# Optimization experiments

Measured on AMD Instinct MI355X. Metric: run time of the kernel, lower is better.

Reference implementation:

```python
import jax, jax.numpy as jnp
import numpy as np

B, C, H, W = 32, 3, 224, 224
P = 16
D = 768
NH = 12
HD = D // NH
DFF = 3072
L = 12
MAXLEN = 256
S = (H // P) * (W // P)  # 196 patches
EPS = 1e-5


def setup_inputs() -> dict:
    key = jax.random.key(0)
    ks = jax.random.split(key, 10)
    r = lambda k, shp, s=0.02: jax.random.normal(k, shp, jnp.float32) * s
    return {
        "x": jax.random.normal(ks[0], (B, C, H, W), jnp.float32),
        "bn_gamma": jnp.ones((C,), jnp.float32),
        "bn_beta": jnp.zeros((C,), jnp.float32),
        "bn_mean": jnp.zeros((C,), jnp.float32),
        "bn_var": jnp.ones((C,), jnp.float32),
        "proj_w": r(ks[1], (P * P * 3, D)),
        "proj_b": jnp.zeros((D,), jnp.float32),
        "cls_w": r(ks[2], (1, D)),
        "Wq": r(ks[3], (L, D, D)),
        "Wk": r(ks[4], (L, D, D)),
        "Wv": r(ks[5], (L, D, D)),
        "fc1_w": r(ks[6], (L, D, DFF)),
        "fc1_b": jnp.zeros((L, DFF), jnp.float32),
        "fc2_w": r(ks[7], (L, DFF, D)),
        "fc2_b": jnp.zeros((L, D), jnp.float32),
        "ln1_g": jnp.ones((L, D), jnp.float32),
        "ln1_b": jnp.zeros((L, D), jnp.float32),
        "ln2_g": jnp.ones((L, D), jnp.float32),
        "ln2_b": jnp.zeros((L, D), jnp.float32),
    }


def _pos_encoding(max_len, d):
    # Faithful to source: exponent is 2*i/d where i is the EVEN index itself.
    pos = jnp.arange(max_len, dtype=jnp.float32)[:, None]
    i = jnp.arange(0, d, 2, dtype=jnp.float32)[None, :]
    ang = pos / (10000.0 ** (2.0 * i / d))
    pe = jnp.zeros((max_len, d), jnp.float32)
    pe = pe.at[:, 0::2].set(jnp.sin(ang))
    pe = pe.at[:, 1::2].set(jnp.cos(ang))
    return pe


def _layernorm(x, g, b):
    m = jnp.mean(x, axis=-1, keepdims=True)
    v = jnp.mean((x - m) ** 2, axis=-1, keepdims=True)
    return (x - m) * jax.lax.rsqrt(v + EPS) * g + b


def reference(x, bn_gamma, bn_beta, bn_mean, bn_var, proj_w, proj_b, cls_w,
              Wq, Wk, Wv, fc1_w, fc1_b, fc2_w, fc2_b,
              ln1_g, ln1_b, ln2_g, ln2_b):
    b = x.shape[0]
    # BatchNorm2d (inference mode, running stats)
    xb = (x - bn_mean[None, :, None, None]) * jax.lax.rsqrt(bn_var[None, :, None, None] + EPS)
    xb = xb * bn_gamma[None, :, None, None] + bn_beta[None, :, None, None]
    # Patchify (nn.Unfold order: channel-major within each patch) -> [B, S, C*P*P]
    patches = xb.reshape(b, C, H // P, P, W // P, P)
    patches = patches.transpose(0, 2, 4, 1, 3, 5).reshape(b, S, C * P * P)
    h = patches @ proj_w + proj_b  # [B, S, D]
    cls = jnp.broadcast_to(cls_w[None], (b, 1, D))
    h = jnp.concatenate([cls, h], axis=1)  # [B, S+1, D]
    pe = _pos_encoding(MAXLEN, D)
    h = h + pe[None, : S + 1, :]
    scale = 1.0 / jnp.sqrt(jnp.float32(HD))
    n = S + 1
    for l in range(L):
        q = (h @ Wq[l]).reshape(b, n, NH, HD).transpose(0, 2, 1, 3)
        k = (h @ Wk[l]).reshape(b, n, NH, HD).transpose(0, 2, 1, 3)
        v = (h @ Wv[l]).reshape(b, n, NH, HD).transpose(0, 2, 1, 3)
        scores = jnp.einsum("bhqd,bhkd->bhqk", q, k) * scale
        attn = jax.nn.softmax(scores, axis=-1)
        att = jnp.einsum("bhqk,bhkd->bhqd", attn, v)  # [B, NH, n, HD]
        # Source bug replicated: direct view [B,NH,n,HD] -> [B,n,D] (no head transpose)
        att = att.reshape(b, n, D)
        h1 = _layernorm(h + att, ln1_g[l], ln1_b[l])
        ff = jax.nn.relu(h1 @ fc1_w[l] + fc1_b[l]) @ fc2_w[l] + fc2_b[l]
        h = _layernorm(h1 + ff, ln2_g[l], ln2_b[l])
    return h[:, 0, :]
```

## Files before the change

### kernel.cpp

```cpp
#include <hip/hip_runtime.h>

typedef unsigned short u16;
typedef __bf16 bf16x8 __attribute__((ext_vector_type(8)));
typedef float f32x4 __attribute__((ext_vector_type(4)));

#define NB 32
#define ND 768
#define NTOK 197
#define NROWS (NB * NTOK)
#define NPATCH 196
#define PROWS (NB * NPATCH)
#define NHD 12
#define NDFF 3072
#define NLAY 12
#define NQKV 2304

static __device__ __forceinline__ u16 f2b(float f) {
  unsigned int u = __builtin_bit_cast(unsigned int, f);
  unsigned int r = u + 0x7FFFu + ((u >> 16) & 1u);
  return (u16)(r >> 16);
}

static __device__ __forceinline__ float wsum(float v) {
#pragma unroll
  for (int off = 32; off > 0; off >>= 1) v += __shfl_xor(v, off);
  return v;
}

static __device__ __forceinline__ void stage16(const u16* g, u16* l) {
  __builtin_amdgcn_global_load_lds((const __attribute__((address_space(1))) void*)g,
                                   (__attribute__((address_space(3))) void*)l, 16, 0, 0);
}

__global__ void pe_kernel(float* __restrict__ pe) {
  int idx = blockIdx.x * 256 + threadIdx.x;
  if (idx >= NTOK * ND) return;
  int t = idx / ND, d = idx % ND;
  int i = d & ~1;
  float e = (2.0f * (float)i) / (float)ND;
  float denom = powf(10000.0f, e);
  float ang = (float)t / denom;
  pe[idx] = (d & 1) ? cosf(ang) : sinf(ang);
}

__global__ void patch_kernel(const float* __restrict__ x,
                             const float* __restrict__ bng, const float* __restrict__ bnb,
                             const float* __restrict__ bnm, const float* __restrict__ bnv,
                             u16* __restrict__ out) {
  int idx = blockIdx.x * 256 + threadIdx.x;
  if (idx >= PROWS * ND) return;
  int row = idx / ND, col = idx % ND;
  int b = row / NPATCH, s = row % NPATCH;
  int ph = s / 14, pw = s % 14;
  int c = col / 256, rr = col % 256;
  int py = rr / 16, px = rr % 16;
  float v = x[(((size_t)(b * 3 + c) * 224) + ph * 16 + py) * 224 + pw * 16 + px];
  v = (v - bnm[c]) * rsqrtf(bnv[c] + 1e-5f) * bng[c] + bnb[c];
  out[idx] = f2b(v);
}

__global__ void cls_kernel(const float* __restrict__ cls_w, const float* __restrict__ pe,
                           float* __restrict__ h, u16* __restrict__ hb) {
  int idx = blockIdx.x * 256 + threadIdx.x;
  if (idx >= NB * ND) return;
  int b = idx / ND, d = idx % ND;
  float v = cls_w[d] + pe[d];
  size_t o = (size_t)(b * NTOK) * ND + d;
  h[o] = v;
  hb[o] = f2b(v);
}

__global__ __launch_bounds__(256) void transpose_cvt(const float* __restrict__ src,
                                                     u16* __restrict__ dst, int R, int C) {
  __shared__ float tile[32][33];
  int tx = threadIdx.x, ty = threadIdx.y;
  int c0 = blockIdx.x * 32, r0 = blockIdx.y * 32;
#pragma unroll
  for (int i = ty; i < 32; i += 8) {
    int r = r0 + i, c = c0 + tx;
    tile[i][tx] = (r < R && c < C) ? src[(size_t)r * C + c] : 0.f;
  }
  __syncthreads();
#pragma unroll
  for (int i = ty; i < 32; i += 8) {
    int c = c0 + i, r = r0 + tx;
    if (r < R && c < C) dst[(size_t)c * R + r] = f2b(tile[tx][i]);
  }
}

__global__ __launch_bounds__(256) void transpose_layer(
    const float* __restrict__ Wq, const float* __restrict__ Wk, const float* __restrict__ Wv,
    const float* __restrict__ f1, const float* __restrict__ f2,
    u16* __restrict__ wqkvt, u16* __restrict__ fc1t, u16* __restrict__ fc2t) {
  int idx = blockIdx.x;
  const float* src;
  u16* dst;
  int C, R, rt, ct;
  if (idx < 1728) {
    int z = idx / 576, loc = idx % 576;
    src = z == 0 ? Wq : (z == 1 ? Wk : Wv);
    dst = wqkvt + (size_t)z * ND * ND;
    R = 768; C = 768; rt = loc / 24; ct = loc % 24;
  } else if (idx < 4032) {
    int loc = idx - 1728;
    src = f1; dst = fc1t; R = 768; C = 3072; rt = loc / 96; ct = loc % 96;
  } else {
    int loc = idx - 4032;
    src = f2; dst = fc2t; R = 3072; C = 768; rt = loc / 24; ct = loc % 24;
  }
  __shared__ float tile[32][33];
  int tx = threadIdx.x & 31, ty = threadIdx.x >> 5;
  int r0 = rt * 32, c0 = ct * 32;
#pragma unroll
  for (int i = ty; i < 32; i += 8) tile[i][tx] = src[(size_t)(r0 + i) * C + c0 + tx];
  __syncthreads();
#pragma unroll
  for (int i = ty; i < 32; i += 8) dst[(size_t)(c0 + i) * R + r0 + tx] = f2b(tile[tx][i]);
}

template <int MODE>
__global__ __launch_bounds__(512, 4) void gemm2(const u16* __restrict__ A,
                                                const u16* __restrict__ Bt,
                                                const float* __restrict__ bias,
                                                const float* __restrict__ pe,
                                                float* __restrict__ Cf, u16* __restrict__ Cb,
                                                int M, int N, int K, int lda, int nby) {
  __shared__ u16 smem[36864];
  const int tid = threadIdx.x;
  const int w = tid >> 6, l = tid & 63;
  const int lr = l & 15, lg = l >> 4;
  const int wr = w >> 1, wc = w & 1;

  const int nwg = gridDim.x;
  const int q8 = nwg >> 3, r8 = nwg & 7;
  const int xcd = blockIdx.x & 7, sidx = blockIdx.x >> 3;
  const int swz = (xcd < r8 ? xcd * (q8 + 1) : r8 * (q8 + 1) + (xcd - r8) * q8) + sidx;
  const int m0 = (swz / nby) * 256, n0 = (swz % nby) * 128;

  A += (size_t)blockIdx.z * K;
  Bt += (size_t)blockIdx.z * K;

  const int srow = l >> 2;
  const int scol = (((l & 3) ^ ((l >> 2) & 3) ^ ((l >> 4) & 3))) * 8;
  int raA0 = m0 + 32 * w + srow;
  int raA1 = raA0 + 16;
  raA0 = raA0 < M ? raA0 : M - 1;
  raA1 = raA1 < M ? raA1 : M - 1;
  const int rbB = n0 + 16 * w + srow;
  const u16* pA0 = A + (size_t)raA0 * lda + scol;
  const u16* pA1 = A + (size_t)raA1 * lda + scol;
  const u16* pB = Bt + (size_t)rbB * lda + scol;
  const int dsgA0 = (2 * w) * 512;
  const int dsgA1 = (2 * w + 1) * 512;
  const int dsgB = 8192 + w * 512;

  const int xo = ((lg ^ (lr & 3) ^ ((lr >> 2) & 3))) * 8;
  const int aoff = (wr * 64 + lr) * 32 + xo;
  const int boff = 8192 + (wc * 64 + lr) * 32 + xo;

  f32x4 acc[4][4] = {};
  const int nk = K >> 5;

#define BARF                           \
  {                                    \
    __builtin_amdgcn_sched_barrier(0); \
    __builtin_amdgcn_s_barrier();      \
    asm volatile("" ::: "memory");     \
    __builtin_amdgcn_sched_barrier(0); \
  }
#define VMW(N) asm volatile("s_waitcnt vmcnt(" #N ")" ::: "memory");

  stage16(pA0, smem + dsgA0);
  stage16(pA1, smem + dsgA1);
  stage16(pB, smem + dsgB);
  stage16(pA0 + 32, smem + 12288 + dsgA0);
  stage16(pA1 + 32, smem + 12288 + dsgA1);
  stage16(pB + 32, smem + 12288 + dsgB);
  VMW(3);
  BARF;

  int cur = 0;
  for (int t = 0; t < nk; ++t) {
    const u16* sb = smem + cur * 12288;
    int c2 = cur + 2;
    if (c2 >= 3) c2 -= 3;
    const bool more2 = (t + 2) < nk;
    if (more2) {
      u16* db = smem + c2 * 12288;
      const int ko = (t + 2) * 32;
      stage16(pA0 + ko, db + dsgA0);
      stage16(pA1 + ko, db + dsgA1);
      stage16(pB + ko, db + dsgB);
    }
    bf16x8 ar[4], br[4];
#pragma unroll
    for (int n = 0; n < 4; ++n) br[n] = *(const bf16x8*)(sb + boff + n * 512);
#pragma unroll
    for (int m = 0; m < 4; ++m) ar[m] = *(const bf16x8*)(sb + aoff + m * 512);
    __builtin_amdgcn_s_setprio(1);
#pragma unroll
    for (int m = 0; m < 4; ++m) {
#pragma unroll
      for (int n = 0; n < 4; ++n)
        acc[m][n] = __builtin_amdgcn_mfma_f32_16x16x32_bf16(ar[m], br[n], acc[m][n], 0, 0, 0);
    }
    __builtin_amdgcn_s_setprio(0);
    if (more2) {
      VMW(3);
    } else if (t + 1 < nk) {
      VMW(0);
    }
    if (t + 1 < nk) BARF;
    cur = cur == 2 ? 0 : cur + 1;
  }

  const size_t zoff = (size_t)blockIdx.z * (size_t)M * (size_t)N;
#pragma unroll
  for (int m = 0; m < 4; ++m) {
    const int rowb = m0 + wr * 64 + m * 16 + lg * 4;
#pragma unroll
    for (int n = 0; n < 4; ++n) {
      const int col = n0 + wc * 64 + n * 16 + lr;
      float bval = (MODE == 0 || MODE == 2) ? bias[col] : 0.f;
#pragma unroll
      for (int r = 0; r < 4; ++r) {
        const int row = rowb + r;
        if (row < M) {
          float v = acc[m][n][r] + bval;
          if (MODE == 2) v = fmaxf(v, 0.f);
          if (MODE == 0) {
            int b = row / NPATCH, t = 1 + row % NPATCH;
            float val = v + pe[(size_t)t * ND + col];
            size_t o = (size_t)(b * NTOK + t) * ND + col;
            Cf[o] = val;
            Cb[o] = f2b(val);
          } else if (MODE == 4) {
            Cf[zoff + (size_t)row * N + col] = v;
          } else {
            Cb[(size_t)row * N + col] = f2b(v);
          }
        }
      }
    }
  }
}

__global__ __launch_bounds__(256) void attn_kernel(const u16* __restrict__ qkv,
                                                   float* __restrict__ att) {
  const int b = blockIdx.x, h = blockIdx.y;
  const int tid = threadIdx.x;
  const int wave = tid >> 6, lane = tid & 63;
  const int lr = lane & 15, lg = lane >> 4;
  __shared__ u16 Vt[64][232];
  __shared__ u16 Pl[4][16][232];

  const size_t bbase = (size_t)(b * NTOK) * NQKV + h * 64;

  for (int idx = tid; idx < NTOK * 64; idx += 256) {
    int k2 = idx >> 6, d = idx & 63;
    Vt[d][k2] = qkv[bbase + (size_t)k2 * NQKV + 1536 + d];
  }
  for (int idx = tid; idx < 64 * 35; idx += 256) {
    int d = idx / 35, k2 = 197 + idx % 35;
    Vt[d][k2] = 0;
  }
  for (int idx = tid; idx < 4 * 16 * 24; idx += 256) {
    int w = idx / (16 * 24), rr = (idx / 24) % 16, c = 208 + idx % 24;
    Pl[w][rr][c] = 0;
  }
  __syncthreads();

  for (int mt = wave; mt < 13; mt += 4) {
    int qrow = mt * 16 + lr;
    if (qrow > 196) qrow = 196;
    bf16x8 af[2];
#pragma unroll
    for (int ks = 0; ks < 2; ks++)
      af[ks] =
          *reinterpret_cast<const bf16x8*>(qkv + bbase + (size_t)qrow * NQKV + ks * 32 + lg * 8);

    f32x4 sf[13];
#pragma unroll
    for (int nt = 0; nt < 13; nt++) {
      int krow = nt * 16 + lr;
      if (krow > 196) krow = 196;
      f32x4 z = {0.f, 0.f, 0.f, 0.f};
#pragma unroll
      for (int ks = 0; ks < 2; ks++) {
        bf16x8 bf_ = *reinterpret_cast<const bf16x8*>(qkv + bbase + (size_t)krow * NQKV + 768 +
                                                      ks * 32 + lg * 8);
        z = __builtin_amdgcn_mfma_f32_16x16x32_bf16(af[ks], bf_, z, 0, 0, 0);
      }
      sf[nt] = z;
    }

    float sm[4];
#pragma unroll
    for (int r = 0; r < 4; r++) {
      float mx = -1e30f;
#pragma unroll
      for (int nt = 0; nt < 13; nt++) {
        int col = nt * 16 + lr;
        float val = (col < NTOK) ? sf[nt][r] * 0.125f : -1e30f;
        sf[nt][r] = val;
        mx = fmaxf(mx, val);
      }
#pragma unroll
      for (int off = 1; off < 16; off <<= 1) mx = fmaxf(mx, __shfl_xor(mx, off));
      float sum = 0.f;
#pragma unroll
      for (int nt = 0; nt < 13; nt++) {
        float pv = __expf(sf[nt][r] - mx);
        sum += pv;
        Pl[wave][lg * 4 + r][nt * 16 + lr] = f2b(pv);
      }
#pragma unroll
      for (int off = 1; off < 16; off <<= 1) sum += __shfl_xor(sum, off);
      sm[r] = sum;
    }

#pragma unroll
    for (int dt = 0; dt < 4; dt++) {
      f32x4 o = {0.f, 0.f, 0.f, 0.f};
#pragma unroll
      for (int ks = 0; ks < 7; ks++) {
        bf16x8 pa = *reinterpret_cast<const bf16x8*>(&Pl[wave][lr][ks * 32 + lg * 8]);
        bf16x8 vv = *reinterpret_cast<const bf16x8*>(&Vt[dt * 16 + lr][ks * 32 + lg * 8]);
        o = __builtin_amdgcn_mfma_f32_16x16x32_bf16(pa, vv, o, 0, 0, 0);
      }
#pragma unroll
      for (int r = 0; r < 4; r++) {
        int q = mt * 16 + lg * 4 + r;
        if (q < NTOK)
          att[(size_t)b * (NTOK * ND) + ((size_t)(h * NTOK + q)) * 64 + dt * 16 + lr] =
              o[r] / sm[r];
      }
    }
  }
}

__global__ __launch_bounds__(256) void ln_kernel(const float* __restrict__ xa,
                                                 const float* __restrict__ xb,
                                                 const float* __restrict__ gw,
                                                 const float* __restrict__ bw,
                                                 float* __restrict__ yf, u16* __restrict__ yb) {
  int row = blockIdx.x, tid = threadIdx.x;
  size_t base = (size_t)row * ND;
  float v[3];
  float s = 0.f;
#pragma unroll
  for (int i = 0; i < 3; i++) {
    int d = tid + i * 256;
    v[i] = xa[base + d] + xb[base + d];
    s += v[i];
  }
  __shared__ float red[4];
  __shared__ float red2[4];
  s = wsum(s);
  if ((tid & 63) == 0) red[tid >> 6] = s;
  __syncthreads();
  float mean = (red[0] + red[1] + red[2] + red[3]) * (1.f / 768.f);
  float q = 0.f;
#pragma unroll
  for (int i = 0; i < 3; i++) {
    float d0 = v[i] - mean;
    q += d0 * d0;
  }
  q = wsum(q);
  if ((tid & 63) == 0) red2[tid >> 6] = q;
  __syncthreads();
  float inv = rsqrtf((red2[0] + red2[1] + red2[2] + red2[3]) * (1.f / 768.f) + 1e-5f);
#pragma unroll
  for (int i = 0; i < 3; i++) {
    int d = tid + i * 256;
    float val = (v[i] - mean) * inv * gw[d] + bw[d];
    yf[base + d] = val;
    yb[base + d] = f2b(val);
  }
}

__global__ __launch_bounds__(256) void ln_fuse2(const float* __restrict__ h1,
                                                const float* __restrict__ parts,
                                                const float* __restrict__ fb,
                                                const float* __restrict__ gw,
                                                const float* __restrict__ bw,
                                                float* __restrict__ yf, u16* __restrict__ yb) {
  const size_t PS = (size_t)NROWS * ND;
  int row = blockIdx.x, tid = threadIdx.x;
  size_t base = (size_t)row * ND;
  float v[3];
  float s = 0.f;
#pragma unroll
  for (int i = 0; i < 3; i++) {
    int d = tid + i * 256;
    v[i] = h1[base + d] + parts[base + d] + parts[PS + base + d] + parts[2 * PS + base + d] +
           fb[d];
    s += v[i];
  }
  __shared__ float red[4];
  __shared__ float red2[4];
  s = wsum(s);
  if ((tid & 63) == 0) red[tid >> 6] = s;
  __syncthreads();
  float mean = (red[0] + red[1] + red[2] + red[3]) * (1.f / 768.f);
  float q = 0.f;
#pragma unroll
  for (int i = 0; i < 3; i++) {
    float d0 = v[i] - mean;
    q += d0 * d0;
  }
  q = wsum(q);
  if ((tid & 63) == 0) red2[tid >> 6] = q;
  __syncthreads();
  float inv = rsqrtf((red2[0] + red2[1] + red2[2] + red2[3]) * (1.f / 768.f) + 1e-5f);
#pragma unroll
  for (int i = 0; i < 3; i++) {
    int d = tid + i * 256;
    float val = (v[i] - mean) * inv * gw[d] + bw[d];
    yf[base + d] = val;
    yb[base + d] = f2b(val);
  }
}

__global__ void outcopy_kernel(const float* __restrict__ h, float* __restrict__ out) {
  int idx = blockIdx.x * 256 + threadIdx.x;
  if (idx >= NB * ND) return;
  int b = idx / ND, d = idx % ND;
  out[idx] = h[(size_t)(b * NTOK) * ND + d];
}

extern "C" void kernel_launch(void* const* d_in, const int* in_sizes, int n_in, void* d_out,
                              int out_size, void* d_ws, size_t ws_size, hipStream_t stream) {
  const float* x = (const float*)d_in[0];
  const float* bng = (const float*)d_in[1];
  const float* bnb = (const float*)d_in[2];
  const float* bnm = (const float*)d_in[3];
  const float* bnv = (const float*)d_in[4];
  const float* proj_w = (const float*)d_in[5];
  const float* proj_b = (const float*)d_in[6];
  const float* cls_w = (const float*)d_in[7];
  const float* Wq = (const float*)d_in[8];
  const float* Wk = (const float*)d_in[9];
  const float* Wv = (const float*)d_in[10];
  const float* fc1_w = (const float*)d_in[11];
  const float* fc1_b = (const float*)d_in[12];
  const float* fc2_w = (const float*)d_in[13];
  const float* fc2_b = (const float*)d_in[14];
  const float* ln1_g = (const float*)d_in[15];
  const float* ln1_b = (const float*)d_in[16];
  const float* ln2_g = (const float*)d_in[17];
  const float* ln2_b = (const float*)d_in[18];

  char* wp = (char*)d_ws;
  auto carve = [&](size_t bytes) -> char* {
    char* r = wp;
    wp += (bytes + 255) & ~(size_t)255;
    return r;
  };
  float* pe = (float*)carve((size_t)NTOK * ND * 4);
  u16* patches = (u16*)carve((size_t)PROWS * ND * 2);
  u16* projwt = (u16*)carve((size_t)ND * ND * 2);
  u16* wqkvt = (u16*)carve((size_t)NQKV * ND * 2);
  u16* fc1t = (u16*)carve((size_t)ND * NDFF * 2);
  u16* fc2t = (u16*)carve((size_t)ND * NDFF * 2);
  float* h = (float*)carve((size_t)NROWS * ND * 4);
  u16* hb = (u16*)carve((size_t)NROWS * ND * 2);
  float* h1 = (float*)carve((size_t)NROWS * ND * 4);
  u16* h1b = (u16*)carve((size_t)NROWS * ND * 2);
  char* uni = carve(3 * (size_t)NROWS * ND * 4);
  u16* qkvb = (u16*)uni;
  float* parts = (float*)uni;
  float* att = (float*)carve((size_t)NROWS * ND * 4);
  u16* ffb = (u16*)carve((size_t)NROWS * NDFF * 2);
  if ((size_t)(wp - (char*)d_ws) > ws_size) return;

  pe_kernel<<<(NTOK * ND + 255) / 256, 256, 0, stream>>>(pe);
  patch_kernel<<<(PROWS * ND + 255) / 256, 256, 0, stream>>>(x, bng, bnb, bnm, bnv, patches);
  transpose_cvt<<<dim3(24, 24), dim3(32, 8), 0, stream>>>(proj_w, projwt, ND, ND);
  gemm2<0><<<dim3(150, 1, 1), 512, 0, stream>>>(patches, projwt, proj_b, pe, h, hb, PROWS, ND,
                                                ND, ND, 6);
  cls_kernel<<<(NB * ND + 255) / 256, 256, 0, stream>>>(cls_w, pe, h, hb);

  for (int l = 0; l < NLAY; ++l) {
    size_t wo = (size_t)l * ND * ND;
    transpose_layer<<<6336, 256, 0, stream>>>(Wq + wo, Wk + wo, Wv + wo,
                                              fc1_w + (size_t)l * ND * NDFF,
                                              fc2_w + (size_t)l * NDFF * ND, wqkvt, fc1t, fc2t);
    gemm2<1><<<dim3(450, 1, 1), 512, 0, stream>>>(hb, wqkvt, nullptr, nullptr, nullptr, qkvb,
                                                  NROWS, NQKV, ND, ND, 18);
    attn_kernel<<<dim3(NB, NHD), 256, 0, stream>>>(qkvb, att);
    ln_kernel<<<NROWS, 256, 0, stream>>>(h, att, ln1_g + l * ND, ln1_b + l * ND, h1, h1b);
    gemm2<2><<<dim3(600, 1, 1), 512, 0, stream>>>(h1b, fc1t, fc1_b + l * NDFF, nullptr, nullptr,
                                                  ffb, NROWS, NDFF, ND, ND, 24);
    gemm2<4><<<dim3(150, 1, 3), 512, 0, stream>>>(ffb, fc2t, nullptr, nullptr, parts, nullptr,
                                                  NROWS, ND, 1024, NDFF, 6);
    ln_fuse2<<<NROWS, 256, 0, stream>>>(h1, parts, fc2_b + l * ND, ln2_g + l * ND, ln2_b + l * ND,
                                        h, hb);
  }
  outcopy_kernel<<<(NB * ND + 255) / 256, 256, 0, stream>>>(h, (float*)d_out);
}
```

Baseline: 2.354 ms.

## Store attention output and split-K partials in bf16; vectorize patch, transpose, and layernorm kernels

Attention output and the three split-K FC2 partial sums are now written as bf16 instead of fp32, which halves their memory traffic. The layernorm kernels are rewritten to use 384 threads, each handling two elements with vector loads. The weight transpose now works on 64x64 tiles with float2 loads and packed bf16 stores, and the patch kernel produces 8 elements per thread. Rounding the split-K partials and the attention output to bf16 before summing adds numerical error.

```diff
diff --git a/kernel.cpp b/kernel.cpp
--- a/kernel.cpp
+++ b/kernel.cpp
@@ -1,8 +1,10 @@
 #include <hip/hip_runtime.h>
 
 typedef unsigned short u16;
+typedef unsigned int u32;
 typedef __bf16 bf16x8 __attribute__((ext_vector_type(8)));
 typedef float f32x4 __attribute__((ext_vector_type(4)));
+typedef u16 u16x8 __attribute__((ext_vector_type(8)));
 
 #define NB 32
 #define ND 768
@@ -16,9 +18,13 @@
 #define NQKV 2304
 
 static __device__ __forceinline__ u16 f2b(float f) {
-  unsigned int u = __builtin_bit_cast(unsigned int, f);
-  unsigned int r = u + 0x7FFFu + ((u >> 16) & 1u);
+  u32 u = __builtin_bit_cast(u32, f);
+  u32 r = u + 0x7FFFu + ((u >> 16) & 1u);
   return (u16)(r >> 16);
+}
+static __device__ __forceinline__ float b2f(u16 u) {
+  u32 x = ((u32)u) << 16;
+  return __builtin_bit_cast(float, x);
 }
 
 static __device__ __forceinline__ float wsum(float v) {
@@ -48,15 +54,20 @@
                              const float* __restrict__ bnm, const float* __restrict__ bnv,
                              u16* __restrict__ out) {
   int idx = blockIdx.x * 256 + threadIdx.x;
-  if (idx >= PROWS * ND) return;
-  int row = idx / ND, col = idx % ND;
+  if (idx >= PROWS * 96) return;
+  int row = idx / 96, c8 = (idx % 96) * 8;
   int b = row / NPATCH, s = row % NPATCH;
   int ph = s / 14, pw = s % 14;
-  int c = col / 256, rr = col % 256;
-  int py = rr / 16, px = rr % 16;
-  float v = x[(((size_t)(b * 3 + c) * 224) + ph * 16 + py) * 224 + pw * 16 + px];
-  v = (v - bnm[c]) * rsqrtf(bnv[c] + 1e-5f) * bng[c] + bnb[c];
-  out[idx] = f2b(v);
+  int c = c8 / 256, rr = c8 % 256;
+  int py = rr / 16, px0 = rr % 16;
+  const float* xp =
+      x + (((size_t)(b * 3 + c) * 224) + ph * 16 + py) * 224 + pw * 16 + px0;
+  float scale = rsqrtf(bnv[c] + 1e-5f) * bng[c];
+  float sub = bnm[c], add = bnb[c];
+  u16x8 o;
+#pragma unroll
+  for (int j = 0; j < 8; j++) o[j] = f2b((xp[j] - sub) * scale + add);
+  *reinterpret_cast<u16x8*>(out + (size_t)idx * 8) = o;
 }
 
 __global__ void cls_kernel(const float* __restrict__ cls_w, const float* __restrict__ pe,
@@ -88,7 +99,7 @@
   }
 }
 
-__global__ __launch_bounds__(256) void transpose_layer(
+__global__ __launch_bounds__(512) void transpose_layer(
     const float* __restrict__ Wq, const float* __restrict__ Wk, const float* __restrict__ Wv,
     const float* __restrict__ f1, const float* __restrict__ f2,
     u16* __restrict__ wqkvt, u16* __restrict__ fc1t, u16* __restrict__ fc2t) {
@@ -96,26 +107,33 @@
   const float* src;
   u16* dst;
   int C, R, rt, ct;
-  if (idx < 1728) {
-    int z = idx / 576, loc = idx % 576;
+  if (idx < 432) {
+    int z = idx / 144, loc = idx % 144;
     src = z == 0 ? Wq : (z == 1 ? Wk : Wv);
     dst = wqkvt + (size_t)z * ND * ND;
-    R = 768; C = 768; rt = loc / 24; ct = loc % 24;
-  } else if (idx < 4032) {
-    int loc = idx - 1728;
-    src = f1; dst = fc1t; R = 768; C = 3072; rt = loc / 96; ct = loc % 96;
+    R = 768; C = 768; rt = loc / 12; ct = loc % 12;
+  } else if (idx < 1008) {
+    int loc = idx - 432;
+    src = f1; dst = fc1t; R = 768; C = 3072; rt = loc / 48; ct = loc % 48;
   } else {
-    int loc = idx - 4032;
-    src = f2; dst = fc2t; R = 3072; C = 768; rt = loc / 24; ct = loc % 24;
-  }
-  __shared__ float tile[32][33];
-  int tx = threadIdx.x & 31, ty = threadIdx.x >> 5;
-  int r0 = rt * 32, c0 = ct * 32;
-#pragma unroll
-  for (int i = ty; i < 32; i += 8) tile[i][tx] = src[(size_t)(r0 + i) * C + c0 + tx];
-  __syncthreads();
-#pragma unroll
-  for (int i = ty; i < 32; i += 8) dst[(size_t)(c0 + i) * R + r0 + tx] = f2b(tile[tx][i]);
+    int loc = idx - 1008;
+    src = f2; dst = fc2t; R = 3072; C = 768; rt = loc / 12; ct = loc % 12;
+  }
+  __shared__ float tile[64][65];
+  const int l2 = threadIdx.x & 31, rp = threadIdx.x >> 5;
+  const int r0 = rt * 64, c0 = ct * 64;
+#pragma unroll
+  for (int i = rp; i < 64; i += 16) {
+    float2 v = *reinterpret_cast<const float2*>(src + (size_t)(r0 + i) * C + c0 + l2 * 2);
+    tile[i][l2 * 2] = v.x;
+    tile[i][l2 * 2 + 1] = v.y;
+  }
+  __syncthreads();
+#pragma unroll
+  for (int j = rp; j < 64; j += 16) {
+    u32 o = (u32)f2b(tile[l2 * 2][j]) | ((u32)f2b(tile[l2 * 2 + 1][j]) << 16);
+    *reinterpret_cast<u32*>(dst + (size_t)(c0 + j) * R + r0 + l2 * 2) = o;
+  }
 }
 
 template <int MODE>
@@ -235,7 +253,7 @@
             Cf[o] = val;
             Cb[o] = f2b(val);
           } else if (MODE == 4) {
-            Cf[zoff + (size_t)row * N + col] = v;
+            Cb[zoff + (size_t)row * N + col] = f2b(v);
           } else {
             Cb[(size_t)row * N + col] = f2b(v);
           }
@@ -246,7 +264,7 @@
 }
 
 __global__ __launch_bounds__(256) void attn_kernel(const u16* __restrict__ qkv,
-                                                   float* __restrict__ att) {
+                                                   u16* __restrict__ att) {
   const int b = blockIdx.x, h = blockIdx.y;
   const int tid = threadIdx.x;
   const int wave = tid >> 6, lane = tid & 63;
@@ -333,93 +351,74 @@
         int q = mt * 16 + lg * 4 + r;
         if (q < NTOK)
           att[(size_t)b * (NTOK * ND) + ((size_t)(h * NTOK + q)) * 64 + dt * 16 + lr] =
-              o[r] / sm[r];
+              f2b(o[r] / sm[r]);
       }
     }
   }
 }
 
-__global__ __launch_bounds__(256) void ln_kernel(const float* __restrict__ xa,
-                                                 const float* __restrict__ xb,
+__global__ __launch_bounds__(384) void ln_kernel(const float* __restrict__ xa,
+                                                 const u16* __restrict__ xb,
                                                  const float* __restrict__ gw,
                                                  const float* __restrict__ bw,
                                                  float* __restrict__ yf, u16* __restrict__ yb) {
   int row = blockIdx.x, tid = threadIdx.x;
-  size_t base = (size_t)row * ND;
-  float v[3];
-  float s = 0.f;
-#pragma unroll
-  for (int i = 0; i < 3; i++) {
-    int d = tid + i * 256;
-    v[i] = xa[base + d] + xb[base + d];
-    s += v[i];
-  }
-  __shared__ float red[4];
-  __shared__ float red2[4];
-  s = wsum(s);
+  size_t p2 = (size_t)row * 384 + tid;
+  float2 a = reinterpret_cast<const float2*>(xa)[p2];
+  u32 bb = reinterpret_cast<const u32*>(xb)[p2];
+  float v0 = a.x + b2f((u16)(bb & 0xffff));
+  float v1 = a.y + b2f((u16)(bb >> 16));
+  __shared__ float red[8], red2[8];
+  float s = wsum(v0 + v1);
   if ((tid & 63) == 0) red[tid >> 6] = s;
   __syncthreads();
-  float mean = (red[0] + red[1] + red[2] + red[3]) * (1.f / 768.f);
-  float q = 0.f;
-#pragma unroll
-  for (int i = 0; i < 3; i++) {
-    float d0 = v[i] - mean;
-    q += d0 * d0;
-  }
-  q = wsum(q);
+  float mean = (red[0] + red[1] + red[2] + red[3] + red[4] + red[5]) * (1.f / 768.f);
+  float d0 = v0 - mean, d1 = v1 - mean;
+  float q = wsum(d0 * d0 + d1 * d1);
   if ((tid & 63) == 0) red2[tid >> 6] = q;
   __syncthreads();
-  float inv = rsqrtf((red2[0] + red2[1] + red2[2] + red2[3]) * (1.f / 768.f) + 1e-5f);
-#pragma unroll
-  for (int i = 0; i < 3; i++) {
-    int d = tid + i * 256;
-    float val = (v[i] - mean) * inv * gw[d] + bw[d];
-    yf[base + d] = val;
-    yb[base + d] = f2b(val);
-  }
-}
-
-__global__ __launch_bounds__(256) void ln_fuse2(const float* __restrict__ h1,
-                                                const float* __restrict__ parts,
+  float inv =
+      rsqrtf((red2[0] + red2[1] + red2[2] + red2[3] + red2[4] + red2[5]) * (1.f / 768.f) + 1e-5f);
+  int d = tid * 2;
+  float o0 = d0 * inv * gw[d] + bw[d];
+  float o1 = d1 * inv * gw[d + 1] + bw[d + 1];
+  float2 of = {o0, o1};
+  reinterpret_cast<float2*>(yf)[p2] = of;
+  reinterpret_cast<u32*>(yb)[p2] = (u32)f2b(o0) | ((u32)f2b(o1) << 16);
+}
+
+__global__ __launch_bounds__(384) void ln_fuse2(const float* __restrict__ h1,
+                                                const u16* __restrict__ parts,
                                                 const float* __restrict__ fb,
                                                 const float* __restrict__ gw,
                                                 const float* __restrict__ bw,
                                                 float* __restrict__ yf, u16* __restrict__ yb) {
-  const size_t PS = (size_t)NROWS * ND;
+  const size_t PS2 = (size_t)NROWS * ND / 2;
   int row = blockIdx.x, tid = threadIdx.x;
-  size_t base = (size_t)row * ND;
-  float v[3];
-  float s = 0.f;
-#pragma unroll
-  for (int i = 0; i < 3; i++) {
-    int d = tid + i * 256;
-    v[i] = h1[base + d] + parts[base + d] + parts[PS + base + d] + parts[2 * PS + base + d] +
-           fb[d];
-    s += v[i];
-  }
-  __shared__ float red[4];
-  __shared__ float red2[4];
-  s = wsum(s);
+  size_t p2 = (size_t)row * 384 + tid;
+  float2 a = reinterpret_cast<const float2*>(h1)[p2];
+  const u32* pp = reinterpret_cast<const u32*>(parts);
+  u32 q0 = pp[p2], q1 = pp[PS2 + p2], q2 = pp[2 * PS2 + p2];
+  int d = tid * 2;
+  float v0 = a.x + b2f((u16)(q0 & 0xffff)) + b2f((u16)(q1 & 0xffff)) + b2f((u16)(q2 & 0xffff)) +
+             fb[d];
+  float v1 = a.y + b2f((u16)(q0 >> 16)) + b2f((u16)(q1 >> 16)) + b2f((u16)(q2 >> 16)) + fb[d + 1];
+  __shared__ float red[8], red2[8];
+  float s = wsum(v0 + v1);
   if ((tid & 63) == 0) red[tid >> 6] = s;
   __syncthreads();
-  float mean = (red[0] + red[1] + red[2] + red[3]) * (1.f / 768.f);
-  float q = 0.f;
-#pragma unroll
-  for (int i = 0; i < 3; i++) {
-    float d0 = v[i] - mean;
-    q += d0 * d0;
-  }
-  q = wsum(q);
+  float mean = (red[0] + red[1] + red[2] + red[3] + red[4] + red[5]) * (1.f / 768.f);
+  float d0 = v0 - mean, d1 = v1 - mean;
+  float q = wsum(d0 * d0 + d1 * d1);
   if ((tid & 63) == 0) red2[tid >> 6] = q;
   __syncthreads();
-  float inv = rsqrtf((red2[0] + red2[1] + red2[2] + red2[3]) * (1.f / 768.f) + 1e-5f);
-#pragma unroll
-  for (int i = 0; i < 3; i++) {
-    int d = tid + i * 256;
-    float val = (v[i] - mean) * inv * gw[d] + bw[d];
-    yf[base + d] = val;
-    yb[base + d] = f2b(val);
-  }
+  float inv =
+      rsqrtf((red2[0] + red2[1] + red2[2] + red2[3] + red2[4] + red2[5]) * (1.f / 768.f) + 1e-5f);
+  float o0 = d0 * inv * gw[d] + bw[d];
+  float o1 = d1 * inv * gw[d + 1] + bw[d + 1];
+  float2 of = {o0, o1};
+  reinterpret_cast<float2*>(yf)[p2] = of;
+  reinterpret_cast<u32*>(yb)[p2] = (u32)f2b(o0) | ((u32)f2b(o1) << 16);
 }
 
 __global__ void outcopy_kernel(const float* __restrict__ h, float* __restrict__ out) {
@@ -467,15 +466,15 @@
   u16* hb = (u16*)carve((size_t)NROWS * ND * 2);
   float* h1 = (float*)carve((size_t)NROWS * ND * 4);
   u16* h1b = (u16*)carve((size_t)NROWS * ND * 2);
-  char* uni = carve(3 * (size_t)NROWS * ND * 4);
+  char* uni = carve(3 * (size_t)NROWS * ND * 2);
   u16* qkvb = (u16*)uni;
-  float* parts = (float*)uni;
-  float* att = (float*)carve((size_t)NROWS * ND * 4);
+  u16* parts = (u16*)uni;
+  u16* att = (u16*)carve((size_t)NROWS * ND * 2);
   u16* ffb = (u16*)carve((size_t)NROWS * NDFF * 2);
   if ((size_t)(wp - (char*)d_ws) > ws_size) return;
 
   pe_kernel<<<(NTOK * ND + 255) / 256, 256, 0, stream>>>(pe);
-  patch_kernel<<<(PROWS * ND + 255) / 256, 256, 0, stream>>>(x, bng, bnb, bnm, bnv, patches);
+  patch_kernel<<<(PROWS * 96 + 255) / 256, 256, 0, stream>>>(x, bng, bnb, bnm, bnv, patches);
   transpose_cvt<<<dim3(24, 24), dim3(32, 8), 0, stream>>>(proj_w, projwt, ND, ND);
   gemm2<0><<<dim3(150, 1, 1), 512, 0, stream>>>(patches, projwt, proj_b, pe, h, hb, PROWS, ND,
                                                 ND, ND, 6);
@@ -483,18 +482,18 @@
 
   for (int l = 0; l < NLAY; ++l) {
     size_t wo = (size_t)l * ND * ND;
-    transpose_layer<<<6336, 256, 0, stream>>>(Wq + wo, Wk + wo, Wv + wo,
+    transpose_layer<<<1584, 512, 0, stream>>>(Wq + wo, Wk + wo, Wv + wo,
                                               fc1_w + (size_t)l * ND * NDFF,
                                               fc2_w + (size_t)l * NDFF * ND, wqkvt, fc1t, fc2t);
     gemm2<1><<<dim3(450, 1, 1), 512, 0, stream>>>(hb, wqkvt, nullptr, nullptr, nullptr, qkvb,
                                                   NROWS, NQKV, ND, ND, 18);
     attn_kernel<<<dim3(NB, NHD), 256, 0, stream>>>(qkvb, att);
-    ln_kernel<<<NROWS, 256, 0, stream>>>(h, att, ln1_g + l * ND, ln1_b + l * ND, h1, h1b);
+    ln_kernel<<<NROWS, 384, 0, stream>>>(h, att, ln1_g + l * ND, ln1_b + l * ND, h1, h1b);
     gemm2<2><<<dim3(600, 1, 1), 512, 0, stream>>>(h1b, fc1t, fc1_b + l * NDFF, nullptr, nullptr,
                                                   ffb, NROWS, NDFF, ND, ND, 24);
-    gemm2<4><<<dim3(150, 1, 3), 512, 0, stream>>>(ffb, fc2t, nullptr, nullptr, parts, nullptr,
+    gemm2<4><<<dim3(150, 1, 3), 512, 0, stream>>>(ffb, fc2t, nullptr, nullptr, nullptr, parts,
                                                   NROWS, ND, 1024, NDFF, 6);
-    ln_fuse2<<<NROWS, 256, 0, stream>>>(h1, parts, fc2_b + l * ND, ln2_g + l * ND, ln2_b + l * ND,
+    ln_fuse2<<<NROWS, 384, 0, stream>>>(h1, parts, fc2_b + l * ND, ln2_g + l * ND, ln2_b + l * ND,
                                         h, hb);
   }
   outcopy_kernel<<<(NB * ND + 255) / 256, 256, 0, stream>>>(h, (float*)d_out);
```

Result: faster. 2.268 ms (-3.6%).
